# Performance work log

Measured on AMD Instinct MI355X. Metric: run time of the kernel, lower is better.

## Reference

```python
import jax, jax.numpy as jnp
import numpy as np

N_NODES = 100000
N_EDGES = 1600000
NEG_SLOPE = 0.2  # PyG GATConv default


def _glorot(key, shape, fan):
    return jax.random.normal(key, shape, dtype=jnp.float32) * np.float32(1.0 / np.sqrt(fan))


def setup_inputs() -> dict:
    key = jax.random.key(0)
    ks = jax.random.split(key, 10)
    x = jax.random.normal(ks[0], (N_NODES, 4), dtype=jnp.float32)
    edge_index = jax.random.randint(ks[1], (2, N_EDGES), 0, N_NODES, dtype=jnp.int32)
    # GAT layer 1: in=4, heads=4, out=16 (concat -> 64)
    W1 = _glorot(ks[2], (4, 64), 4)
    a_src1 = _glorot(ks[3], (4, 16), 16)
    a_dst1 = _glorot(ks[4], (4, 16), 16)
    b1 = jnp.zeros((64,), jnp.float32)
    # GAT layer 2: in=64, heads=2, out=8 (concat -> 16)
    W2 = _glorot(ks[5], (64, 16), 64)
    a_src2 = _glorot(ks[6], (2, 8), 8)
    a_dst2 = _glorot(ks[7], (2, 8), 8)
    b2 = jnp.zeros((16,), jnp.float32)
    lin_w = _glorot(ks[8], (16, 1), 16)
    lin_b = jnp.zeros((1,), jnp.float32)
    return {
        "x": x, "edge_index": edge_index,
        "W1": W1, "a_src1": a_src1, "a_dst1": a_dst1, "b1": b1,
        "W2": W2, "a_src2": a_src2, "a_dst2": a_dst2, "b2": b2,
        "lin_w": lin_w, "lin_b": lin_b,
    }


def gat_layer(x, src, dst, W, a_src, a_dst, b, heads, out_dim):
    """PyG GATConv (concat=True, add_self_loops=True). src -> dst messages."""
    n = x.shape[0]
    h = (x @ W).reshape(n, heads, out_dim)          # [N,H,D]
    al_s = jnp.sum(h * a_src, axis=-1)              # [N,H]
    al_d = jnp.sum(h * a_dst, axis=-1)              # [N,H]
    loop = jnp.arange(n, dtype=src.dtype)
    src_f = jnp.concatenate([src, loop])            # [E+N]
    dst_f = jnp.concatenate([dst, loop])
    e = jax.nn.leaky_relu(al_s[src_f] + al_d[dst_f], NEG_SLOPE)  # [E+N,H]
    # numerically-stable segment softmax over incoming edges of each dst node
    m = jax.lax.stop_gradient(jax.ops.segment_max(e, dst_f, num_segments=n))
    ex = jnp.exp(e - m[dst_f])
    denom = jax.ops.segment_sum(ex, dst_f, num_segments=n)
    alpha = ex / (denom[dst_f] + 1e-16)             # [E+N,H]
    msg = h[src_f] * alpha[..., None]               # [E+N,H,D]
    out = jax.ops.segment_sum(msg, dst_f, num_segments=n)  # [N,H,D]
    return out.reshape(n, heads * out_dim) + b


def reference(x, edge_index, W1, a_src1, a_dst1, b1, W2, a_src2, a_dst2, b2, lin_w, lin_b):
    # dropout is identity at inference time
    src, dst = edge_index[0], edge_index[1]
    h = gat_layer(x, src, dst, W1, a_src1, a_dst1, b1, heads=4, out_dim=16)
    h = jax.nn.elu(h)
    h = gat_layer(h, src, dst, W2, a_src2, a_dst2, b2, heads=2, out_dim=8)
    h = jax.nn.elu(h)
    return jax.nn.sigmoid(h @ lin_w + lin_b)        # [N,1]
```

## Files before the change

### kernel.cpp

```cpp
#include <hip/hip_runtime.h>
#include <math.h>


#define NEG_SLOPE 0.2f
#define SHIFT 8
#define BN 256
#define BMASK 255
#define CAPB 8192
#define STCAP 6144

__device__ __forceinline__ float lrelu(float v) { return v >= 0.f ? v : NEG_SLOPE * v; }

__global__ void kb_scatter(const int* __restrict__ src, const int* __restrict__ dst,
                           int* __restrict__ bcur, unsigned* __restrict__ ebuf, int E) {
    __shared__ int lh[512], lbase[512], loff[512];
    int t = threadIdx.x;
    lh[t] = 0; lh[t + 256] = 0;
    __syncthreads();
    const int4* src4 = reinterpret_cast<const int4*>(src);
    const int4* dst4 = reinterpret_cast<const int4*>(dst);
    int base4 = blockIdx.x * 1024;
    int myb[16];
    unsigned myv[16];
#pragma unroll
    for (int it = 0; it < 4; ++it) {
        int i4 = base4 + it * 256 + t;
        if (i4 * 4 < E) {
            int4 s4 = src4[i4], d4 = dst4[i4];
            int ss[4] = {s4.x, s4.y, s4.z, s4.w};
            int dd[4] = {d4.x, d4.y, d4.z, d4.w};
#pragma unroll
            for (int c = 0; c < 4; ++c) {
                int b = dd[c] >> SHIFT;
                myb[it * 4 + c] = b;
                myv[it * 4 + c] = (unsigned)ss[c] | ((unsigned)(dd[c] & BMASK) << 17);
                atomicAdd(&lh[b], 1);
            }
        } else {
#pragma unroll
            for (int c = 0; c < 4; ++c) myb[it * 4 + c] = -1;
        }
    }
    __syncthreads();
    if (lh[t]) lbase[t] = atomicAdd(&bcur[t], lh[t]);
    if (lh[t + 256]) lbase[t + 256] = atomicAdd(&bcur[t + 256], lh[t + 256]);
    loff[t] = 0; loff[t + 256] = 0;
    __syncthreads();
#pragma unroll
    for (int it = 0; it < 16; ++it) {
        int b = myb[it];
        if (b >= 0) {
            int o = lbase[b] + atomicAdd(&loff[b], 1);
            if (o < CAPB) ebuf[(size_t)b * CAPB + o] = myv[it];
        }
    }
}

__global__ void __launch_bounds__(512) kbA1(
        const float* __restrict__ x, const float* __restrict__ W1,
        const float* __restrict__ as1, const float* __restrict__ ad1,
        const float* __restrict__ b1, const float* __restrict__ W2,
        const float* __restrict__ as2, const float* __restrict__ ad2,
        const int* __restrict__ bcur, const unsigned* __restrict__ ebuf,
        float* __restrict__ h2, float* __restrict__ als2, float* __restrict__ ald2, int N)
{
    __shared__ float sW[256], swals[16], swald[16], sb1[64], sW2[1024], sas2[16], sad2[16];
    __shared__ float aldL[BN * 5];
    __shared__ int nh[BN], ns[BN], stmp[BN];
    __shared__ int stage[STCAP];
    __shared__ float sE[128 * 65];
    int t = threadIdx.x, b = blockIdx.x;
    if (t < 256) { sW[t] = W1[t]; nh[t] = 0; }
    for (int i = t; i < 1024; i += 512) sW2[i] = W2[i];
    if (t < 64) sb1[t] = b1[t];
    if (t >= 64 && t < 80) { sas2[t - 64] = as2[t - 64]; sad2[t - 64] = ad2[t - 64]; }
    __syncthreads();
    if (t < 16) {
        int head = t >> 2, i = t & 3;
        float s1 = 0.f, s2 = 0.f;
        for (int d = 0; d < 16; ++d) {
            float w = sW[i * 64 + head * 16 + d];
            s1 += w * as1[head * 16 + d];
            s2 += w * ad1[head * 16 + d];
        }
        swals[t] = s1;
        swald[t] = s2;
    }
    __syncthreads();

    int node0 = b << SHIFT;
    int nn = min(BN, N - node0);
    const float4* x4 = reinterpret_cast<const float4*>(x);
    int ne = min(bcur[b], STCAP);
    const unsigned* eb = ebuf + (size_t)b * CAPB;

    for (int i = t; i < ne; i += 512) atomicAdd(&nh[eb[i] >> 17], 1);
    for (int j = t; j < nn; j += 512) {
        float4 xd = x4[node0 + j];
#pragma unroll
        for (int h = 0; h < 4; ++h)
            aldL[j * 5 + h] = xd.x * swald[h * 4 + 0] + xd.y * swald[h * 4 + 1]
                            + xd.z * swald[h * 4 + 2] + xd.w * swald[h * 4 + 3];
    }
    __syncthreads();

    int vcnt = 0;
    if (t < 256) { vcnt = nh[t]; stmp[t] = vcnt; }
    __syncthreads();
#pragma unroll
    for (int off = 1; off < 256; off <<= 1) {
        int a = 0;
        if (t < 256 && t >= off) a = stmp[t - off];
        __syncthreads();
        if (t < 256) stmp[t] += a;
        __syncthreads();
    }
    if (t < 256) ns[t] = stmp[t] - vcnt;
    __syncthreads();

    for (int i = t; i < ne; i += 512) {
        unsigned pk = eb[i];
        int pos = atomicAdd(&ns[pk >> 17], 1);
        stage[pos] = (int)(pk & 0x1FFFFu);
    }
    __syncthreads();

    int g = t >> 2, tt = t & 3;
    float wa0 = swals[tt * 4 + 0], wa1 = swals[tt * 4 + 1];
    float wa2 = swals[tt * 4 + 2], wa3 = swals[tt * 4 + 3];
#pragma unroll
    for (int c = 0; c < 2; ++c) {
        int j = c * 128 + g;
        int n = node0 + j;
        bool act = j < nn;
        int e = act ? nh[j] : 0;
        int st = act ? (ns[j] - e) : 0;
        float aldv = act ? aldL[j * 5 + tt] : 0.f;
        float dA = 0.f, aA0 = 0.f, aA1 = 0.f, aA2 = 0.f, aA3 = 0.f;
        float dB = 0.f, aB0 = 0.f, aB1 = 0.f, aB2 = 0.f, aB3 = 0.f;
        int h = e >> 1;
        for (int i = 0; i < h; ++i) {
            int sA = stage[st + i];
            int sB = stage[st + h + i];
            float4 xA = x4[sA];
            float4 xB = x4[sB];
            float vA = lrelu(fmaf(xA.x, wa0, fmaf(xA.y, wa1, fmaf(xA.z, wa2, fmaf(xA.w, wa3, aldv)))));
            float vB = lrelu(fmaf(xB.x, wa0, fmaf(xB.y, wa1, fmaf(xB.z, wa2, fmaf(xB.w, wa3, aldv)))));
            float pA = __expf(vA);
            float pB = __expf(vB);
            dA += pA;                  dB += pB;
            aA0 = fmaf(pA, xA.x, aA0); aB0 = fmaf(pB, xB.x, aB0);
            aA1 = fmaf(pA, xA.y, aA1); aB1 = fmaf(pB, xB.y, aB1);
            aA2 = fmaf(pA, xA.z, aA2); aB2 = fmaf(pB, xB.z, aB2);
            aA3 = fmaf(pA, xA.w, aA3); aB3 = fmaf(pB, xB.w, aB3);
        }
        if (e & 1) {
            int s = stage[st + e - 1];
            float4 xs = x4[s];
            float v = lrelu(fmaf(xs.x, wa0, fmaf(xs.y, wa1, fmaf(xs.z, wa2, fmaf(xs.w, wa3, aldv)))));
            float p = __expf(v);
            dA += p;
            aA0 = fmaf(p, xs.x, aA0); aA1 = fmaf(p, xs.y, aA1);
            aA2 = fmaf(p, xs.z, aA2); aA3 = fmaf(p, xs.w, aA3);
        }
        float4 xn = act ? x4[n] : make_float4(0.f, 0.f, 0.f, 0.f);
        float als_s = xn.x * wa0 + xn.y * wa1 + xn.z * wa2 + xn.w * wa3;
        float ps = __expf(lrelu(als_s + aldv));
        float inv = 1.f / (dA + dB + ps + 1e-16f);
        float a0 = (aA0 + aB0 + ps * xn.x) * inv;
        float a1 = (aA1 + aB1 + ps * xn.y) * inv;
        float a2 = (aA2 + aB2 + ps * xn.z) * inv;
        float a3 = (aA3 + aB3 + ps * xn.w) * inv;

#pragma unroll
        for (int d = 0; d < 16; ++d) {
            int col = tt * 16 + d;
            float v = a0 * sW[col] + a1 * sW[64 + col] + a2 * sW[128 + col]
                    + a3 * sW[192 + col] + sb1[col];
            sE[g * 65 + col] = v > 0.f ? v : expm1f(v);
        }
        float o0 = 0.f, o1 = 0.f, o2 = 0.f, o3 = 0.f;
#pragma unroll
        for (int k = 0; k < 64; ++k) {
            float ev = sE[g * 65 + k];
            o0 = fmaf(ev, sW2[k * 16 + tt * 4 + 0], o0);
            o1 = fmaf(ev, sW2[k * 16 + tt * 4 + 1], o1);
            o2 = fmaf(ev, sW2[k * 16 + tt * 4 + 2], o2);
            o3 = fmaf(ev, sW2[k * 16 + tt * 4 + 3], o3);
        }
        if (act)
            reinterpret_cast<float4*>(h2)[(size_t)n * 4 + tt] = make_float4(o0, o1, o2, o3);
        int head2 = tt >> 1, half = tt & 1;
        const float* s2p = sas2 + head2 * 8 + half * 4;
        const float* d2p = sad2 + head2 * 8 + half * 4;
        float qs = o0 * s2p[0] + o1 * s2p[1] + o2 * s2p[2] + o3 * s2p[3];
        float qd = o0 * d2p[0] + o1 * d2p[1] + o2 * d2p[2] + o3 * d2p[3];
        qs += __shfl_xor(qs, 1);
        qd += __shfl_xor(qd, 1);
        if (act && half == 0) {
            als2[n * 2 + head2] = qs;
            ald2[n * 2 + head2] = qd;
        }
    }
}

__global__ void __launch_bounds__(512) kbA2(
        const float* __restrict__ h2, const float* __restrict__ als2,
        const float* __restrict__ ald2, const float* __restrict__ b2,
        const float* __restrict__ lw, const float* __restrict__ lb,
        const int* __restrict__ bcur, const unsigned* __restrict__ ebuf,
        float* __restrict__ out, int N)
{
    __shared__ int nh[BN], ns[BN], stmp[BN];
    __shared__ int stage[STCAP];
    __shared__ float ald2L[BN * 2];
    __shared__ float sb2[16], slw[16];
    int t = threadIdx.x, b = blockIdx.x;
    if (t < 256) nh[t] = 0;
    if (t < 16) { sb2[t] = b2[t]; slw[t] = lw[t]; }
    int node0 = b << SHIFT;
    int nn = min(BN, N - node0);
    __syncthreads();
    int ne = min(bcur[b], STCAP);
    const unsigned* eb = ebuf + (size_t)b * CAPB;
    for (int i = t; i < ne; i += 512) atomicAdd(&nh[eb[i] >> 17], 1);
    for (int j = t; j < nn * 2; j += 512) ald2L[j] = ald2[node0 * 2 + j];
    __syncthreads();
    int vcnt = 0;
    if (t < 256) { vcnt = nh[t]; stmp[t] = vcnt; }
    __syncthreads();
#pragma unroll
    for (int off = 1; off < 256; off <<= 1) {
        int a = 0;
        if (t < 256 && t >= off) a = stmp[t - off];
        __syncthreads();
        if (t < 256) stmp[t] += a;
        __syncthreads();
    }
    if (t < 256) ns[t] = stmp[t] - vcnt;
    __syncthreads();
    for (int i = t; i < ne; i += 512) {
        unsigned pk = eb[i];
        int pos = atomicAdd(&ns[pk >> 17], 1);
        stage[pos] = (int)(pk & 0x1FFFFu);
    }
    __syncthreads();

    int g = t >> 2, tt = t & 3, head = tt >> 1;
    const float4* h4 = reinterpret_cast<const float4*>(h2);
    const float2* als22 = reinterpret_cast<const float2*>(als2);
#pragma unroll
    for (int c = 0; c < 2; ++c) {
        int j = c * 128 + g;
        int n = node0 + j;
        bool act = j < nn;
        int e = act ? nh[j] : 0;
        int st = act ? (ns[j] - e) : 0;
        float aldv = act ? ald2L[j * 2 + head] : 0.f;
        float dA = 0.f, aA0 = 0.f, aA1 = 0.f, aA2 = 0.f, aA3 = 0.f;
        float dB = 0.f, aB0 = 0.f, aB1 = 0.f, aB2 = 0.f, aB3 = 0.f;
        int h = e >> 1;
        for (int i = 0; i < h; ++i) {
            int sA = stage[st + i];
            int sB = stage[st + h + i];
            float2 avA = als22[sA];
            float2 avB = als22[sB];
            float vA = lrelu((head ? avA.y : avA.x) + aldv);
            float vB = lrelu((head ? avB.y : avB.x) + aldv);
            float4 hA = h4[(size_t)sA * 4 + tt];
            float4 hB = h4[(size_t)sB * 4 + tt];
            float pA = __expf(vA);
            float pB = __expf(vB);
            dA += pA;                  dB += pB;
            aA0 = fmaf(pA, hA.x, aA0); aB0 = fmaf(pB, hB.x, aB0);
            aA1 = fmaf(pA, hA.y, aA1); aB1 = fmaf(pB, hB.y, aB1);
            aA2 = fmaf(pA, hA.z, aA2); aB2 = fmaf(pB, hB.z, aB2);
            aA3 = fmaf(pA, hA.w, aA3); aB3 = fmaf(pB, hB.w, aB3);
        }
        if (e & 1) {
            int s = stage[st + e - 1];
            float2 av = als22[s];
            float v = lrelu((head ? av.y : av.x) + aldv);
            float4 hs = h4[(size_t)s * 4 + tt];
            float p = __expf(v);
            dA += p;
            aA0 = fmaf(p, hs.x, aA0); aA1 = fmaf(p, hs.y, aA1);
            aA2 = fmaf(p, hs.z, aA2); aA3 = fmaf(p, hs.w, aA3);
        }
        float dot = 0.f;
        if (act) {
            float2 av = als22[n];
            float ps = __expf(lrelu((head ? av.y : av.x) + aldv));
            float4 hn = h4[(size_t)n * 4 + tt];
            float inv = 1.f / (dA + dB + ps + 1e-16f);
            float v0 = (aA0 + aB0 + ps * hn.x) * inv + sb2[tt * 4 + 0];
            float v1 = (aA1 + aB1 + ps * hn.y) * inv + sb2[tt * 4 + 1];
            float v2 = (aA2 + aB2 + ps * hn.z) * inv + sb2[tt * 4 + 2];
            float v3 = (aA3 + aB3 + ps * hn.w) * inv + sb2[tt * 4 + 3];
            v0 = v0 > 0.f ? v0 : expm1f(v0);
            v1 = v1 > 0.f ? v1 : expm1f(v1);
            v2 = v2 > 0.f ? v2 : expm1f(v2);
            v3 = v3 > 0.f ? v3 : expm1f(v3);
            dot = v0 * slw[tt * 4 + 0] + v1 * slw[tt * 4 + 1]
                + v2 * slw[tt * 4 + 2] + v3 * slw[tt * 4 + 3];
        }
        dot += __shfl_xor(dot, 1);
        dot += __shfl_xor(dot, 2);
        if (act && tt == 0) out[n] = 1.f / (1.f + __expf(-(dot + lb[0])));
    }
}

extern "C" void kernel_launch(void* const* d_in, const int* in_sizes, int n_in,
                              void* d_out, int out_size, void* d_ws, size_t ws_size,
                              hipStream_t stream) {
    const float* x     = (const float*)d_in[0];
    const int*   eidx  = (const int*)d_in[1];
    const float* W1    = (const float*)d_in[2];
    const float* as1   = (const float*)d_in[3];
    const float* ad1   = (const float*)d_in[4];
    const float* b1    = (const float*)d_in[5];
    const float* W2    = (const float*)d_in[6];
    const float* as2   = (const float*)d_in[7];
    const float* ad2   = (const float*)d_in[8];
    const float* b2    = (const float*)d_in[9];
    const float* lin_w = (const float*)d_in[10];
    const float* lin_b = (const float*)d_in[11];
    float* out = (float*)d_out;

    const int N = in_sizes[0] / 4;
    const int E = in_sizes[1] / 2;
    const int* src = eidx;
    const int* dst = eidx + E;
    const int NB = (N + BMASK) >> SHIFT;

    int*      bcur = (int*)d_ws;
    unsigned* ebuf = (unsigned*)(bcur + 512);
    float*    h2   = (float*)(ebuf + (size_t)NB * CAPB);
    float*    als2 = h2 + (size_t)N * 16;
    float*    ald2 = als2 + (size_t)N * 2;

    hipMemsetAsync(bcur, 0, 512 * sizeof(int), stream);
    kb_scatter<<<(E + 4095) / 4096, 256, 0, stream>>>(src, dst, bcur, ebuf, E);
    kbA1<<<NB, 512, 0, stream>>>(x, W1, as1, ad1, b1, W2, as2, ad2,
                                 bcur, ebuf, h2, als2, ald2, N);
    kbA2<<<NB, 512, 0, stream>>>(h2, als2, ald2, b2, lin_w, lin_b,
                                 bcur, ebuf, out, N);
}
```

Baseline: 163.8 us.

## Persist CSR from layer-1 kernel and split edges across lanes per node

Layer-1 kernel now writes its locally sorted per-block edge lists, per-node counts and row starts to global memory, so the layer-2 kernel no longer re-histograms, prefix-scans and re-buckets edges in shared memory. Both aggregation loops are changed so the four lanes of a node stride over its edges and each computes all heads, followed by shuffle reductions. Before, each lane handled one head over every edge. This aims to spread work over high-degree nodes and cut redundant index loads. The cost is extra global writes and reads for the CSR, more registers, and more shuffles.

```diff
diff --git a/kernel.cpp b/kernel.cpp
--- a/kernel.cpp
+++ b/kernel.cpp
@@ -10,6 +10,10 @@
 #define STCAP 6144
 
 __device__ __forceinline__ float lrelu(float v) { return v >= 0.f ? v : NEG_SLOPE * v; }
+__device__ __forceinline__ float sel4(int tt, float v0, float v1, float v2, float v3) {
+    return tt == 0 ? v0 : tt == 1 ? v1 : tt == 2 ? v2 : v3;
+}
+#define RED4(v) { v += __shfl_xor(v, 1); v += __shfl_xor(v, 2); }
 
 __global__ void kb_scatter(const int* __restrict__ src, const int* __restrict__ dst,
                            int* __restrict__ bcur, unsigned* __restrict__ ebuf, int E) {
@@ -62,6 +66,7 @@
         const float* __restrict__ b1, const float* __restrict__ W2,
         const float* __restrict__ as2, const float* __restrict__ ad2,
         const int* __restrict__ bcur, const unsigned* __restrict__ ebuf,
+        int* __restrict__ csr, int* __restrict__ cnt, int* __restrict__ rstart,
         float* __restrict__ h2, float* __restrict__ als2, float* __restrict__ ald2, int N)
 {
     __shared__ float sW[256], swals[16], swald[16], sb1[64], sW2[1024], sas2[16], sad2[16];
@@ -125,9 +130,23 @@
     }
     __syncthreads();
 
+    {
+        int lim4 = ne & ~3;
+        const int4* st4 = reinterpret_cast<const int4*>(stage);
+        int4* c4 = reinterpret_cast<int4*>(csr + (size_t)b * CAPB);
+        for (int i = t; i * 4 < lim4; i += 512) c4[i] = st4[i];
+        for (int i = lim4 + t; i < ne; i += 512) csr[(size_t)b * CAPB + i] = stage[i];
+        for (int j = t; j < nn; j += 512) {
+            cnt[node0 + j] = nh[j];
+            rstart[node0 + j] = b * CAPB + ns[j] - nh[j];
+        }
+    }
+
     int g = t >> 2, tt = t & 3;
-    float wa0 = swals[tt * 4 + 0], wa1 = swals[tt * 4 + 1];
-    float wa2 = swals[tt * 4 + 2], wa3 = swals[tt * 4 + 3];
+    float wa00 = swals[0],  wa01 = swals[1],  wa02 = swals[2],  wa03 = swals[3];
+    float wa10 = swals[4],  wa11 = swals[5],  wa12 = swals[6],  wa13 = swals[7];
+    float wa20 = swals[8],  wa21 = swals[9],  wa22 = swals[10], wa23 = swals[11];
+    float wa30 = swals[12], wa31 = swals[13], wa32 = swals[14], wa33 = swals[15];
 #pragma unroll
     for (int c = 0; c < 2; ++c) {
         int j = c * 128 + g;
@@ -135,42 +154,54 @@
         bool act = j < nn;
         int e = act ? nh[j] : 0;
         int st = act ? (ns[j] - e) : 0;
+        float al0 = act ? aldL[j * 5 + 0] : 0.f;
+        float al1 = act ? aldL[j * 5 + 1] : 0.f;
+        float al2 = act ? aldL[j * 5 + 2] : 0.f;
+        float al3 = act ? aldL[j * 5 + 3] : 0.f;
+        float dn0 = 0.f, dn1 = 0.f, dn2 = 0.f, dn3 = 0.f;
+        float a00 = 0.f, a01 = 0.f, a02 = 0.f, a03 = 0.f;
+        float a10 = 0.f, a11 = 0.f, a12 = 0.f, a13 = 0.f;
+        float a20 = 0.f, a21 = 0.f, a22 = 0.f, a23 = 0.f;
+        float a30 = 0.f, a31 = 0.f, a32 = 0.f, a33 = 0.f;
+        for (int i = tt; i < e; i += 4) {
+            int s = stage[st + i];
+            float4 xs = x4[s];
+            float v0 = lrelu(fmaf(xs.x, wa00, fmaf(xs.y, wa01, fmaf(xs.z, wa02, fmaf(xs.w, wa03, al0)))));
+            float v1 = lrelu(fmaf(xs.x, wa10, fmaf(xs.y, wa11, fmaf(xs.z, wa12, fmaf(xs.w, wa13, al1)))));
+            float v2 = lrelu(fmaf(xs.x, wa20, fmaf(xs.y, wa21, fmaf(xs.z, wa22, fmaf(xs.w, wa23, al2)))));
+            float v3 = lrelu(fmaf(xs.x, wa30, fmaf(xs.y, wa31, fmaf(xs.z, wa32, fmaf(xs.w, wa33, al3)))));
+            float p0 = __expf(v0), p1 = __expf(v1), p2 = __expf(v2), p3 = __expf(v3);
+            dn0 += p0; dn1 += p1; dn2 += p2; dn3 += p3;
+            a00 = fmaf(p0, xs.x, a00); a01 = fmaf(p0, xs.y, a01);
+            a02 = fmaf(p0, xs.z, a02); a03 = fmaf(p0, xs.w, a03);
+            a10 = fmaf(p1, xs.x, a10); a11 = fmaf(p1, xs.y, a11);
+            a12 = fmaf(p1, xs.z, a12); a13 = fmaf(p1, xs.w, a13);
+            a20 = fmaf(p2, xs.x, a20); a21 = fmaf(p2, xs.y, a21);
+            a22 = fmaf(p2, xs.z, a22); a23 = fmaf(p2, xs.w, a23);
+            a30 = fmaf(p3, xs.x, a30); a31 = fmaf(p3, xs.y, a31);
+            a32 = fmaf(p3, xs.z, a32); a33 = fmaf(p3, xs.w, a33);
+        }
+        RED4(dn0) RED4(dn1) RED4(dn2) RED4(dn3)
+        RED4(a00) RED4(a01) RED4(a02) RED4(a03)
+        RED4(a10) RED4(a11) RED4(a12) RED4(a13)
+        RED4(a20) RED4(a21) RED4(a22) RED4(a23)
+        RED4(a30) RED4(a31) RED4(a32) RED4(a33)
+        float den = sel4(tt, dn0, dn1, dn2, dn3);
+        float s0  = sel4(tt, a00, a10, a20, a30);
+        float s1  = sel4(tt, a01, a11, a21, a31);
+        float s2  = sel4(tt, a02, a12, a22, a32);
+        float s3  = sel4(tt, a03, a13, a23, a33);
+        float4 xn = act ? x4[n] : make_float4(0.f, 0.f, 0.f, 0.f);
+        float wb0 = swals[tt * 4 + 0], wb1 = swals[tt * 4 + 1];
+        float wb2 = swals[tt * 4 + 2], wb3 = swals[tt * 4 + 3];
         float aldv = act ? aldL[j * 5 + tt] : 0.f;
-        float dA = 0.f, aA0 = 0.f, aA1 = 0.f, aA2 = 0.f, aA3 = 0.f;
-        float dB = 0.f, aB0 = 0.f, aB1 = 0.f, aB2 = 0.f, aB3 = 0.f;
-        int h = e >> 1;
-        for (int i = 0; i < h; ++i) {
-            int sA = stage[st + i];
-            int sB = stage[st + h + i];
-            float4 xA = x4[sA];
-            float4 xB = x4[sB];
-            float vA = lrelu(fmaf(xA.x, wa0, fmaf(xA.y, wa1, fmaf(xA.z, wa2, fmaf(xA.w, wa3, aldv)))));
-            float vB = lrelu(fmaf(xB.x, wa0, fmaf(xB.y, wa1, fmaf(xB.z, wa2, fmaf(xB.w, wa3, aldv)))));
-            float pA = __expf(vA);
-            float pB = __expf(vB);
-            dA += pA;                  dB += pB;
-            aA0 = fmaf(pA, xA.x, aA0); aB0 = fmaf(pB, xB.x, aB0);
-            aA1 = fmaf(pA, xA.y, aA1); aB1 = fmaf(pB, xB.y, aB1);
-            aA2 = fmaf(pA, xA.z, aA2); aB2 = fmaf(pB, xB.z, aB2);
-            aA3 = fmaf(pA, xA.w, aA3); aB3 = fmaf(pB, xB.w, aB3);
-        }
-        if (e & 1) {
-            int s = stage[st + e - 1];
-            float4 xs = x4[s];
-            float v = lrelu(fmaf(xs.x, wa0, fmaf(xs.y, wa1, fmaf(xs.z, wa2, fmaf(xs.w, wa3, aldv)))));
-            float p = __expf(v);
-            dA += p;
-            aA0 = fmaf(p, xs.x, aA0); aA1 = fmaf(p, xs.y, aA1);
-            aA2 = fmaf(p, xs.z, aA2); aA3 = fmaf(p, xs.w, aA3);
-        }
-        float4 xn = act ? x4[n] : make_float4(0.f, 0.f, 0.f, 0.f);
-        float als_s = xn.x * wa0 + xn.y * wa1 + xn.z * wa2 + xn.w * wa3;
+        float als_s = xn.x * wb0 + xn.y * wb1 + xn.z * wb2 + xn.w * wb3;
         float ps = __expf(lrelu(als_s + aldv));
-        float inv = 1.f / (dA + dB + ps + 1e-16f);
-        float a0 = (aA0 + aB0 + ps * xn.x) * inv;
-        float a1 = (aA1 + aB1 + ps * xn.y) * inv;
-        float a2 = (aA2 + aB2 + ps * xn.z) * inv;
-        float a3 = (aA3 + aB3 + ps * xn.w) * inv;
+        float inv = 1.f / (den + ps + 1e-16f);
+        float a0 = (s0 + ps * xn.x) * inv;
+        float a1 = (s1 + ps * xn.y) * inv;
+        float a2 = (s2 + ps * xn.z) * inv;
+        float a3 = (s3 + ps * xn.w) * inv;
 
 #pragma unroll
         for (int d = 0; d < 16; ++d) {
@@ -208,95 +239,74 @@
         const float* __restrict__ h2, const float* __restrict__ als2,
         const float* __restrict__ ald2, const float* __restrict__ b2,
         const float* __restrict__ lw, const float* __restrict__ lb,
-        const int* __restrict__ bcur, const unsigned* __restrict__ ebuf,
-        float* __restrict__ out, int N)
+        const int* __restrict__ csr, const int* __restrict__ cnt,
+        const int* __restrict__ rstart, float* __restrict__ out, int N)
 {
-    __shared__ int nh[BN], ns[BN], stmp[BN];
-    __shared__ int stage[STCAP];
     __shared__ float ald2L[BN * 2];
     __shared__ float sb2[16], slw[16];
     int t = threadIdx.x, b = blockIdx.x;
-    if (t < 256) nh[t] = 0;
     if (t < 16) { sb2[t] = b2[t]; slw[t] = lw[t]; }
     int node0 = b << SHIFT;
     int nn = min(BN, N - node0);
-    __syncthreads();
-    int ne = min(bcur[b], STCAP);
-    const unsigned* eb = ebuf + (size_t)b * CAPB;
-    for (int i = t; i < ne; i += 512) atomicAdd(&nh[eb[i] >> 17], 1);
     for (int j = t; j < nn * 2; j += 512) ald2L[j] = ald2[node0 * 2 + j];
     __syncthreads();
-    int vcnt = 0;
-    if (t < 256) { vcnt = nh[t]; stmp[t] = vcnt; }
-    __syncthreads();
-#pragma unroll
-    for (int off = 1; off < 256; off <<= 1) {
-        int a = 0;
-        if (t < 256 && t >= off) a = stmp[t - off];
-        __syncthreads();
-        if (t < 256) stmp[t] += a;
-        __syncthreads();
-    }
-    if (t < 256) ns[t] = stmp[t] - vcnt;
-    __syncthreads();
-    for (int i = t; i < ne; i += 512) {
-        unsigned pk = eb[i];
-        int pos = atomicAdd(&ns[pk >> 17], 1);
-        stage[pos] = (int)(pk & 0x1FFFFu);
-    }
-    __syncthreads();
-
-    int g = t >> 2, tt = t & 3, head = tt >> 1;
+
     const float4* h4 = reinterpret_cast<const float4*>(h2);
     const float2* als22 = reinterpret_cast<const float2*>(als2);
+    int g = t >> 2, tt = t & 3;
 #pragma unroll
     for (int c = 0; c < 2; ++c) {
         int j = c * 128 + g;
         int n = node0 + j;
         bool act = j < nn;
-        int e = act ? nh[j] : 0;
-        int st = act ? (ns[j] - e) : 0;
-        float aldv = act ? ald2L[j * 2 + head] : 0.f;
-        float dA = 0.f, aA0 = 0.f, aA1 = 0.f, aA2 = 0.f, aA3 = 0.f;
-        float dB = 0.f, aB0 = 0.f, aB1 = 0.f, aB2 = 0.f, aB3 = 0.f;
-        int h = e >> 1;
-        for (int i = 0; i < h; ++i) {
-            int sA = stage[st + i];
-            int sB = stage[st + h + i];
-            float2 avA = als22[sA];
-            float2 avB = als22[sB];
-            float vA = lrelu((head ? avA.y : avA.x) + aldv);
-            float vB = lrelu((head ? avB.y : avB.x) + aldv);
-            float4 hA = h4[(size_t)sA * 4 + tt];
-            float4 hB = h4[(size_t)sB * 4 + tt];
-            float pA = __expf(vA);
-            float pB = __expf(vB);
-            dA += pA;                  dB += pB;
-            aA0 = fmaf(pA, hA.x, aA0); aB0 = fmaf(pB, hB.x, aB0);
-            aA1 = fmaf(pA, hA.y, aA1); aB1 = fmaf(pB, hB.y, aB1);
-            aA2 = fmaf(pA, hA.z, aA2); aB2 = fmaf(pB, hB.z, aB2);
-            aA3 = fmaf(pA, hA.w, aA3); aB3 = fmaf(pB, hB.w, aB3);
-        }
-        if (e & 1) {
-            int s = stage[st + e - 1];
+        int e = act ? cnt[n] : 0;
+        int st = act ? rstart[n] : 0;
+        float al0 = act ? ald2L[j * 2 + 0] : 0.f;
+        float al1 = act ? ald2L[j * 2 + 1] : 0.f;
+        float d0 = 0.f, d1 = 0.f;
+        float c0 = 0.f, c1 = 0.f, c2 = 0.f, c3 = 0.f;
+        float c4v = 0.f, c5 = 0.f, c6 = 0.f, c7 = 0.f;
+        float c8 = 0.f, c9 = 0.f, c10 = 0.f, c11 = 0.f;
+        float c12 = 0.f, c13 = 0.f, c14 = 0.f, c15 = 0.f;
+        for (int i = tt; i < e; i += 4) {
+            int s = csr[st + i];
             float2 av = als22[s];
-            float v = lrelu((head ? av.y : av.x) + aldv);
-            float4 hs = h4[(size_t)s * 4 + tt];
-            float p = __expf(v);
-            dA += p;
-            aA0 = fmaf(p, hs.x, aA0); aA1 = fmaf(p, hs.y, aA1);
-            aA2 = fmaf(p, hs.z, aA2); aA3 = fmaf(p, hs.w, aA3);
-        }
+            float p0 = __expf(lrelu(av.x + al0));
+            float p1 = __expf(lrelu(av.y + al1));
+            float4 hA = h4[(size_t)s * 4 + 0], hB = h4[(size_t)s * 4 + 1];
+            float4 hC = h4[(size_t)s * 4 + 2], hD = h4[(size_t)s * 4 + 3];
+            d0 += p0; d1 += p1;
+            c0  = fmaf(p0, hA.x, c0);  c1  = fmaf(p0, hA.y, c1);
+            c2  = fmaf(p0, hA.z, c2);  c3  = fmaf(p0, hA.w, c3);
+            c4v = fmaf(p0, hB.x, c4v); c5  = fmaf(p0, hB.y, c5);
+            c6  = fmaf(p0, hB.z, c6);  c7  = fmaf(p0, hB.w, c7);
+            c8  = fmaf(p1, hC.x, c8);  c9  = fmaf(p1, hC.y, c9);
+            c10 = fmaf(p1, hC.z, c10); c11 = fmaf(p1, hC.w, c11);
+            c12 = fmaf(p1, hD.x, c12); c13 = fmaf(p1, hD.y, c13);
+            c14 = fmaf(p1, hD.z, c14); c15 = fmaf(p1, hD.w, c15);
+        }
+        RED4(d0) RED4(d1)
+        RED4(c0) RED4(c1) RED4(c2) RED4(c3)
+        RED4(c4v) RED4(c5) RED4(c6) RED4(c7)
+        RED4(c8) RED4(c9) RED4(c10) RED4(c11)
+        RED4(c12) RED4(c13) RED4(c14) RED4(c15)
+        float t0 = sel4(tt, c0, c4v, c8,  c12);
+        float t1 = sel4(tt, c1, c5,  c9,  c13);
+        float t2 = sel4(tt, c2, c6,  c10, c14);
+        float t3 = sel4(tt, c3, c7,  c11, c15);
+        float den = (tt < 2) ? d0 : d1;
         float dot = 0.f;
         if (act) {
             float2 av = als22[n];
-            float ps = __expf(lrelu((head ? av.y : av.x) + aldv));
+            float aldv = (tt < 2) ? al0 : al1;
+            float avh = (tt < 2) ? av.x : av.y;
+            float ps = __expf(lrelu(avh + aldv));
             float4 hn = h4[(size_t)n * 4 + tt];
-            float inv = 1.f / (dA + dB + ps + 1e-16f);
-            float v0 = (aA0 + aB0 + ps * hn.x) * inv + sb2[tt * 4 + 0];
-            float v1 = (aA1 + aB1 + ps * hn.y) * inv + sb2[tt * 4 + 1];
-            float v2 = (aA2 + aB2 + ps * hn.z) * inv + sb2[tt * 4 + 2];
-            float v3 = (aA3 + aB3 + ps * hn.w) * inv + sb2[tt * 4 + 3];
+            float inv = 1.f / (den + ps + 1e-16f);
+            float v0 = (t0 + ps * hn.x) * inv + sb2[tt * 4 + 0];
+            float v1 = (t1 + ps * hn.y) * inv + sb2[tt * 4 + 1];
+            float v2 = (t2 + ps * hn.z) * inv + sb2[tt * 4 + 2];
+            float v3 = (t3 + ps * hn.w) * inv + sb2[tt * 4 + 3];
             v0 = v0 > 0.f ? v0 : expm1f(v0);
             v1 = v1 > 0.f ? v1 : expm1f(v1);
             v2 = v2 > 0.f ? v2 : expm1f(v2);
@@ -333,16 +343,19 @@
     const int* dst = eidx + E;
     const int NB = (N + BMASK) >> SHIFT;
 
-    int*      bcur = (int*)d_ws;
-    unsigned* ebuf = (unsigned*)(bcur + 512);
-    float*    h2   = (float*)(ebuf + (size_t)NB * CAPB);
-    float*    als2 = h2 + (size_t)N * 16;
-    float*    ald2 = als2 + (size_t)N * 2;
+    int*      bcur   = (int*)d_ws;
+    unsigned* ebuf   = (unsigned*)(bcur + 512);
+    int*      csr    = (int*)(ebuf + (size_t)NB * CAPB);
+    int*      cnt    = csr + (size_t)NB * CAPB;
+    int*      rstart = cnt + N;
+    float*    h2     = (float*)(rstart + N);
+    float*    als2   = h2 + (size_t)N * 16;
+    float*    ald2   = als2 + (size_t)N * 2;
 
     hipMemsetAsync(bcur, 0, 512 * sizeof(int), stream);
     kb_scatter<<<(E + 4095) / 4096, 256, 0, stream>>>(src, dst, bcur, ebuf, E);
     kbA1<<<NB, 512, 0, stream>>>(x, W1, as1, ad1, b1, W2, as2, ad2,
-                                 bcur, ebuf, h2, als2, ald2, N);
+                                 bcur, ebuf, csr, cnt, rstart, h2, als2, ald2, N);
     kbA2<<<NB, 512, 0, stream>>>(h2, als2, ald2, b2, lin_w, lin_b,
-                                 bcur, ebuf, out, N);
-}
+                                 csr, cnt, rstart, out, N);
+}
```

New measurement: 168.5 us. 1.03x slower.
